# Performance work log

Measured on AMD Instinct MI355X. Metric: run time of the kernel, lower is better.

Reference implementation:

```python
import jax, jax.numpy as jnp
import numpy as np
from jax import lax


def setup_inputs() -> dict:
    key = jax.random.key(0)
    k1, k2 = jax.random.split(key)
    B, C, H, W = 4, 64, 64, 64
    foreground = jax.random.normal(k1, (B, C, H, W), dtype=jnp.float32)
    masks = jax.random.uniform(k2, (B, 1, H, W), dtype=jnp.float32)
    return {"foreground": foreground, "masks": masks}


def reference(foreground, masks):
    # First-call path of KnowledgeConsistentAttention (att_scores_prev is None).
    # patch_size=3 -> padding=1 around 1x1 dynamic kernels; propagate_size=3 -> 3x3 sum pool.
    B, C, H, W = foreground.shape
    P = H * W
    # Dynamic 1x1 kernels: one per spatial location, L2-normalized over channels.
    K = foreground.reshape(B, C, P).transpose(0, 2, 1)            # [B, P, C]
    norm = jnp.sqrt(jnp.sum(K * K, axis=2, keepdims=True))        # flatten(1).norm per kernel
    K = K / (norm + 1e-8)
    # conv2d with 1x1 kernels and padding=1 == GEMM over zero-padded input.
    Xpad = jnp.pad(foreground, ((0, 0), (0, 0), (1, 1), (1, 1)))  # [B, C, H+2, W+2]
    scores = jnp.einsum('bpc,bchw->bphw', K, Xpad)                # [B, P, H+2, W+2]
    # avg_pool2d(k=3, stride=1, pad=1) * 9 == zero-padded 3x3 sum pool.
    scores = lax.reduce_window(scores, jnp.float32(0.0), lax.add,
                               (1, 1, 3, 3), (1, 1, 1, 1), 'SAME')
    attn = jax.nn.softmax(scores, axis=1)                          # softmax over P kernels
    # conv_transpose2d with 1x1 kernels, padding=1 crops the border back to HxW.
    out = jnp.einsum('bphw,bpc->bchw', attn[:, :, 1:-1, 1:-1], K)  # [B, C, H, W]
    return out
```

## Files before the change

### kernel.cpp

```cpp
#include <hip/hip_runtime.h>
#include <hip/hip_bf16.h>
#include <math.h>

#define Bn 4
#define Cn 64
#define Pn 4096
#define QT 32
#define PBK 128
#define NITER (Pn / PBK)
#define LOG2E 1.4426950408889634f

typedef __attribute__((ext_vector_type(8))) short short8;
typedef __attribute__((ext_vector_type(4))) float float4v;
typedef unsigned short bfu;

__device__ __forceinline__ bfu f2bf(float x) {
    unsigned u = __float_as_uint(x);
    u = (u + 0x7fffu + ((u >> 16) & 1u)) >> 16;
    return (bfu)u;
}

__device__ __forceinline__ void async_load16(const bfu* g, bfu* l) {
    __builtin_amdgcn_global_load_lds(
        (const __attribute__((address_space(1))) unsigned int*)(const void*)g,
        (__attribute__((address_space(3))) unsigned int*)(void*)l,
        16, 0, 0);
}

__global__ __launch_bounds__(256) void prep_kernel(const float* __restrict__ fg,
                                                   bfu* __restrict__ Kpc,
                                                   bfu* __restrict__ Kcp,
                                                   float* __restrict__ S) {
    __shared__ float shbuf[64 * 64];
    int t = threadIdx.x;
    if (blockIdx.x < 512) {
        float* tile  = shbuf;
        float* rnorm = shbuf + 64 * 33;
        int b  = blockIdx.x >> 7;
        int p0 = (blockIdx.x & 127) << 5;
        const float* src = fg + (size_t)b * Cn * Pn + p0;
        #pragma unroll
        for (int i = 0; i < 8; ++i) {
            int idx = i * 256 + t;
            int c = idx >> 5, p = idx & 31;
            tile[c * 33 + p] = src[(size_t)c * Pn + p];
        }
        __syncthreads();
        if (t < 32) {
            float ss = 0.f;
            #pragma unroll
            for (int c = 0; c < 64; ++c) { float v = tile[c * 33 + t]; ss += v * v; }
            rnorm[t] = 1.0f / (sqrtf(ss) + 1e-8f);
        }
        __syncthreads();
        bfu* dpc = Kpc + ((size_t)b * Pn + p0) * Cn;
        #pragma unroll
        for (int i = 0; i < 8; ++i) {
            int idx = i * 256 + t;
            int p = idx >> 6, c = idx & 63;
            dpc[(size_t)p * Cn + c] = f2bf(tile[c * 33 + p] * rnorm[p]);
        }
        bfu* dcp = Kcp + (size_t)b * Cn * Pn + p0;
        #pragma unroll
        for (int i = 0; i < 8; ++i) {
            int idx = i * 256 + t;
            int c = idx >> 5, p = idx & 31;
            dcp[(size_t)c * Pn + p] = f2bf(tile[c * 33 + p] * rnorm[p]);
        }
    } else {
        float (*pl)[64] = (float(*)[64])shbuf;
        int bc = blockIdx.x - 512;
        const float* src = fg + (size_t)bc * Pn;
        float*       dst = S  + (size_t)bc * Pn;
        #pragma unroll
        for (int i = 0; i < 16; ++i) {
            int idx = i * 256 + t;
            pl[idx >> 6][idx & 63] = src[idx];
        }
        __syncthreads();
        #pragma unroll
        for (int i = 0; i < 16; ++i) {
            int idx = i * 256 + t;
            int h = idx >> 6, w = idx & 63;
            float s = 0.f;
            #pragma unroll
            for (int dh = -1; dh <= 1; ++dh) {
                int hh = h + dh;
                if (hh < 0 || hh >= 64) continue;
                #pragma unroll
                for (int dw = -1; dw <= 1; ++dw) {
                    int ww = w + dw;
                    if (ww < 0 || ww >= 64) continue;
                    s += pl[hh][ww];
                }
            }
            dst[idx] = s * LOG2E;
        }
    }
}

__global__ __launch_bounds__(256, 2) void flash_kernel(const bfu* __restrict__ Kpc,
                                                       const bfu* __restrict__ Kcp,
                                                       const float* __restrict__ S,
                                                       float* __restrict__ out) {
    __shared__ bfu Kpc_l[2][PBK * 64];
    __shared__ bfu Kcp_l[2][Cn * PBK];
    __shared__ bfu Sl[QT * 64];
    __shared__ bfu El[QT * PBK];
    __shared__ float wredl[4][QT];

    int b  = blockIdx.x >> 7;
    int q0 = (blockIdx.x & 127) * QT;
    int t  = threadIdx.x;
    int w = t >> 6, l = t & 63, lq = l & 15, quad = l >> 4;

    const float* Sg  = S   + (size_t)b * Cn * Pn;
    const bfu*   gpc = Kpc + (size_t)b * Pn * Cn;
    const bfu*   gcp = Kcp + (size_t)b * Cn * Pn;

    {
        int c = t >> 2, qq = (t & 3) * 8;
        const float* sp = &Sg[(size_t)c * Pn + q0 + qq];
        float4 v0 = *(const float4*)sp;
        float4 v1 = *(const float4*)(sp + 4);
        float vv[8] = {v0.x, v0.y, v0.z, v0.w, v1.x, v1.y, v1.z, v1.w};
        int ch = c >> 3, cl = c & 7;
        #pragma unroll
        for (int i = 0; i < 8; ++i) {
            int row = qq + i;
            Sl[row * 64 + ((ch ^ (row & 7)) << 3) + cl] = f2bf(vv[i]);
        }
    }

    #pragma unroll
    for (int j = 0; j < 4; ++j) {
        int ci = (w * 4 + j) * 64 + l;
        int row = ci >> 3, chp = ci & 7;
        async_load16(gpc + (size_t)row * Cn + ((chp ^ (row & 7)) << 3),
                     &Kpc_l[0][(w * 4 + j) * 512]);
    }
    #pragma unroll
    for (int j = 0; j < 4; ++j) {
        int ci = (w * 4 + j) * 64 + l;
        int c = ci >> 4, chp = ci & 15;
        async_load16(gcp + (size_t)c * Pn + ((chp ^ (c & 15)) << 3),
                     &Kcp_l[0][(w * 4 + j) * 512]);
    }
    __syncthreads();

    short8 bs[2][2];
    #pragma unroll
    for (int nt = 0; nt < 2; ++nt)
        #pragma unroll
        for (int ks = 0; ks < 2; ++ks) {
            int row = nt * 16 + lq;
            bs[nt][ks] = *(const short8*)&Sl[row * 64 + (((ks * 4 + quad) ^ (lq & 7)) << 3)];
        }

    float4v o[2];
    o[0] = (float4v){0.f, 0.f, 0.f, 0.f};
    o[1] = (float4v){0.f, 0.f, 0.f, 0.f};
    float lacc[2] = {0.f, 0.f};

    for (int pb = 0; pb < NITER; ++pb) {
        int cur = pb & 1;

        if (pb + 1 < NITER) {
            int nxt = cur ^ 1;
            const bfu* gpc_n = gpc + (size_t)(pb + 1) * PBK * Cn;
            const bfu* gcp_n = gcp + (size_t)(pb + 1) * PBK;
            #pragma unroll
            for (int j = 0; j < 4; ++j) {
                int ci = (w * 4 + j) * 64 + l;
                int row = ci >> 3, chp = ci & 7;
                async_load16(gpc_n + (size_t)row * Cn + ((chp ^ (row & 7)) << 3),
                             &Kpc_l[nxt][(w * 4 + j) * 512]);
            }
            #pragma unroll
            for (int j = 0; j < 4; ++j) {
                int ci = (w * 4 + j) * 64 + l;
                int c = ci >> 4, chp = ci & 15;
                async_load16(gcp_n + (size_t)c * Pn + ((chp ^ (c & 15)) << 3),
                             &Kcp_l[nxt][(w * 4 + j) * 512]);
            }
        }

        short8 af[2][2];
        #pragma unroll
        for (int mt = 0; mt < 2; ++mt)
            #pragma unroll
            for (int ks = 0; ks < 2; ++ks) {
                int row = w * 32 + mt * 16 + lq;
                af[mt][ks] = *(const short8*)&Kpc_l[cur][row * 64 + (((ks * 4 + quad) ^ (lq & 7)) << 3)];
            }
        float4v sc[2][2];
        #pragma unroll
        for (int mt = 0; mt < 2; ++mt)
            #pragma unroll
            for (int nt = 0; nt < 2; ++nt) {
                float4v acc = (float4v){0.f, 0.f, 0.f, 0.f};
                acc = __builtin_amdgcn_mfma_f32_16x16x32_bf16(af[mt][0], bs[nt][0], acc, 0, 0, 0);
                acc = __builtin_amdgcn_mfma_f32_16x16x32_bf16(af[mt][1], bs[nt][1], acc, 0, 0, 0);
                sc[mt][nt] = acc;
            }

        #pragma unroll
        for (int nt = 0; nt < 2; ++nt) {
            int row = nt * 16 + lq;
            #pragma unroll
            for (int mt = 0; mt < 2; ++mt) {
                float e0 = __builtin_amdgcn_exp2f(sc[mt][nt][0]);
                float e1 = __builtin_amdgcn_exp2f(sc[mt][nt][1]);
                float e2 = __builtin_amdgcn_exp2f(sc[mt][nt][2]);
                float e3 = __builtin_amdgcn_exp2f(sc[mt][nt][3]);
                lacc[nt] += (e0 + e1) + (e2 + e3);
                __hip_bfloat162 h01 = __float22bfloat162_rn(make_float2(e0, e1));
                __hip_bfloat162 h23 = __float22bfloat162_rn(make_float2(e2, e3));
                uint2 pk = make_uint2(*(unsigned*)&h01, *(unsigned*)&h23);
                int col = w * 32 + mt * 16 + quad * 4;
                int ch = (col >> 3) ^ (row & 15), cl = col & 7;
                *(uint2*)&El[row * PBK + ch * 8 + cl] = pk;
            }
        }
        __syncthreads();

        #pragma unroll
        for (int ks = 0; ks < 4; ++ks) {
            int rowA = w * 16 + lq;
            short8 ak = *(const short8*)&Kcp_l[cur][rowA * PBK + (((ks * 4 + quad) ^ lq) << 3)];
            #pragma unroll
            for (int nt = 0; nt < 2; ++nt) {
                int rowB = nt * 16 + lq;
                short8 bk = *(const short8*)&El[rowB * PBK + (((ks * 4 + quad) ^ lq) << 3)];
                o[nt] = __builtin_amdgcn_mfma_f32_16x16x32_bf16(ak, bk, o[nt], 0, 0, 0);
            }
        }
        __syncthreads();
    }

    #pragma unroll
    for (int nt = 0; nt < 2; ++nt) {
        lacc[nt] += __shfl_xor(lacc[nt], 16);
        lacc[nt] += __shfl_xor(lacc[nt], 32);
    }
    if (quad == 0) { wredl[w][lq] = lacc[0]; wredl[w][16 + lq] = lacc[1]; }
    __syncthreads();
    float* og = out + (size_t)b * Cn * Pn;
    #pragma unroll
    for (int nt = 0; nt < 2; ++nt) {
        int q = nt * 16 + lq;
        float linv = 1.0f / ((wredl[0][q] + wredl[1][q]) + (wredl[2][q] + wredl[3][q]));
        #pragma unroll
        for (int r = 0; r < 4; ++r) {
            int c = w * 16 + quad * 4 + r;
            og[(size_t)c * Pn + q0 + q] = o[nt][r] * linv;
        }
    }
}

extern "C" void kernel_launch(void* const* d_in, const int* in_sizes, int n_in,
                              void* d_out, int out_size, void* d_ws, size_t ws_size,
                              hipStream_t stream) {
    const float* fg = (const float*)d_in[0];
    float* out = (float*)d_out;
    bfu*   Kpc = (bfu*)d_ws;
    bfu*   Kcp = Kpc + (size_t)Bn * Pn * Cn;
    float* S   = (float*)(Kcp + (size_t)Bn * Pn * Cn);

    prep_kernel <<<768, 256, 0, stream>>>(fg, Kpc, Kcp, S);
    flash_kernel<<<Bn * 128, 256, 0, stream>>>(Kpc, Kcp, S, out);
}
```

Before: 107.1 us.

## Keep softmax probabilities in registers via shuffles, split-K PV across waves

Result: slower. 115.7 us (+8.0%).

```diff
diff --git a/kernel.cpp b/kernel.cpp
--- a/kernel.cpp
+++ b/kernel.cpp
@@ -103,11 +103,9 @@
                                                        const bfu* __restrict__ Kcp,
                                                        const float* __restrict__ S,
                                                        float* __restrict__ out) {
-    __shared__ bfu Kpc_l[2][PBK * 64];
-    __shared__ bfu Kcp_l[2][Cn * PBK];
-    __shared__ bfu Sl[QT * 64];
-    __shared__ bfu El[QT * PBK];
+    __shared__ __align__(16) bfu smem[2 * PBK * 64 + 2 * Cn * PBK + QT * 64];
     __shared__ float wredl[4][QT];
+    bfu* Sl = smem + 2 * PBK * 64 + 2 * Cn * PBK;
 
     int b  = blockIdx.x >> 7;
     int q0 = (blockIdx.x & 127) * QT;
@@ -137,14 +135,14 @@
         int ci = (w * 4 + j) * 64 + l;
         int row = ci >> 3, chp = ci & 7;
         async_load16(gpc + (size_t)row * Cn + ((chp ^ (row & 7)) << 3),
-                     &Kpc_l[0][(w * 4 + j) * 512]);
+                     smem + (w * 4 + j) * 512);
     }
     #pragma unroll
     for (int j = 0; j < 4; ++j) {
         int ci = (w * 4 + j) * 64 + l;
         int c = ci >> 4, chp = ci & 15;
         async_load16(gcp + (size_t)c * Pn + ((chp ^ (c & 15)) << 3),
-                     &Kcp_l[0][(w * 4 + j) * 512]);
+                     smem + 2 * PBK * 64 + (w * 4 + j) * 512);
     }
     __syncthreads();
 
@@ -157,16 +155,24 @@
             bs[nt][ks] = *(const short8*)&Sl[row * 64 + (((ks * 4 + quad) ^ (lq & 7)) << 3)];
         }
 
-    float4v o[2];
-    o[0] = (float4v){0.f, 0.f, 0.f, 0.f};
-    o[1] = (float4v){0.f, 0.f, 0.f, 0.f};
+    float4v o[4][2];
+    #pragma unroll
+    for (int ct = 0; ct < 4; ++ct)
+        #pragma unroll
+        for (int nt = 0; nt < 2; ++nt) o[ct][nt] = (float4v){0.f, 0.f, 0.f, 0.f};
     float lacc[2] = {0.f, 0.f};
 
+    int s0 = ((quad & 1) * 2) * 16 + lq;
+    int s1 = s0 + 16;
+    bool hi = quad >= 2;
+
     for (int pb = 0; pb < NITER; ++pb) {
-        int cur = pb & 1;
+        bfu* KpcC = smem + (pb & 1) * (PBK * 64);
+        bfu* KcpC = smem + 2 * PBK * 64 + (pb & 1) * (Cn * PBK);
 
         if (pb + 1 < NITER) {
-            int nxt = cur ^ 1;
+            bfu* KpcN = smem + ((pb + 1) & 1) * (PBK * 64);
+            bfu* KcpN = smem + 2 * PBK * 64 + ((pb + 1) & 1) * (Cn * PBK);
             const bfu* gpc_n = gpc + (size_t)(pb + 1) * PBK * Cn;
             const bfu* gcp_n = gcp + (size_t)(pb + 1) * PBK;
             #pragma unroll
@@ -174,14 +180,14 @@
                 int ci = (w * 4 + j) * 64 + l;
                 int row = ci >> 3, chp = ci & 7;
                 async_load16(gpc_n + (size_t)row * Cn + ((chp ^ (row & 7)) << 3),
-                             &Kpc_l[nxt][(w * 4 + j) * 512]);
+                             KpcN + (w * 4 + j) * 512);
             }
             #pragma unroll
             for (int j = 0; j < 4; ++j) {
                 int ci = (w * 4 + j) * 64 + l;
                 int c = ci >> 4, chp = ci & 15;
                 async_load16(gcp_n + (size_t)c * Pn + ((chp ^ (c & 15)) << 3),
-                             &Kcp_l[nxt][(w * 4 + j) * 512]);
+                             KcpN + (w * 4 + j) * 512);
             }
         }
 
@@ -191,7 +197,7 @@
             #pragma unroll
             for (int ks = 0; ks < 2; ++ks) {
                 int row = w * 32 + mt * 16 + lq;
-                af[mt][ks] = *(const short8*)&Kpc_l[cur][row * 64 + (((ks * 4 + quad) ^ (lq & 7)) << 3)];
+                af[mt][ks] = *(const short8*)&KpcC[row * 64 + (((ks * 4 + quad) ^ (lq & 7)) << 3)];
             }
         float4v sc[2][2];
         #pragma unroll
@@ -204,9 +210,9 @@
                 sc[mt][nt] = acc;
             }
 
-        #pragma unroll
-        for (int nt = 0; nt < 2; ++nt) {
-            int row = nt * 16 + lq;
+        unsigned pk[2][2][2];
+        #pragma unroll
+        for (int nt = 0; nt < 2; ++nt)
             #pragma unroll
             for (int mt = 0; mt < 2; ++mt) {
                 float e0 = __builtin_amdgcn_exp2f(sc[mt][nt][0]);
@@ -216,24 +222,37 @@
                 lacc[nt] += (e0 + e1) + (e2 + e3);
                 __hip_bfloat162 h01 = __float22bfloat162_rn(make_float2(e0, e1));
                 __hip_bfloat162 h23 = __float22bfloat162_rn(make_float2(e2, e3));
-                uint2 pk = make_uint2(*(unsigned*)&h01, *(unsigned*)&h23);
-                int col = w * 32 + mt * 16 + quad * 4;
-                int ch = (col >> 3) ^ (row & 15), cl = col & 7;
-                *(uint2*)&El[row * PBK + ch * 8 + cl] = pk;
-            }
-        }
-        __syncthreads();
-
-        #pragma unroll
-        for (int ks = 0; ks < 4; ++ks) {
-            int rowA = w * 16 + lq;
-            short8 ak = *(const short8*)&Kcp_l[cur][rowA * PBK + (((ks * 4 + quad) ^ lq) << 3)];
-            #pragma unroll
-            for (int nt = 0; nt < 2; ++nt) {
-                int rowB = nt * 16 + lq;
-                short8 bk = *(const short8*)&El[rowB * PBK + (((ks * 4 + quad) ^ lq) << 3)];
-                o[nt] = __builtin_amdgcn_mfma_f32_16x16x32_bf16(ak, bk, o[nt], 0, 0, 0);
-            }
+                pk[mt][nt][0] = *(unsigned*)&h01;
+                pk[mt][nt][1] = *(unsigned*)&h23;
+            }
+
+        short8 eb[2];
+        #pragma unroll
+        for (int nt = 0; nt < 2; ++nt) {
+            unsigned a, bq;
+            uint4 bw;
+            a  = (unsigned)__shfl((int)pk[0][nt][0], s0);
+            bq = (unsigned)__shfl((int)pk[1][nt][0], s0);
+            bw.x = hi ? bq : a;
+            a  = (unsigned)__shfl((int)pk[0][nt][1], s0);
+            bq = (unsigned)__shfl((int)pk[1][nt][1], s0);
+            bw.y = hi ? bq : a;
+            a  = (unsigned)__shfl((int)pk[0][nt][0], s1);
+            bq = (unsigned)__shfl((int)pk[1][nt][0], s1);
+            bw.z = hi ? bq : a;
+            a  = (unsigned)__shfl((int)pk[0][nt][1], s1);
+            bq = (unsigned)__shfl((int)pk[1][nt][1], s1);
+            bw.w = hi ? bq : a;
+            eb[nt] = *(short8*)&bw;
+        }
+
+        #pragma unroll
+        for (int ct = 0; ct < 4; ++ct) {
+            int row = ct * 16 + lq;
+            short8 ak = *(const short8*)&KcpC[row * PBK + (((4 * w + quad) ^ (row & 15)) << 3)];
+            #pragma unroll
+            for (int nt = 0; nt < 2; ++nt)
+                o[ct][nt] = __builtin_amdgcn_mfma_f32_16x16x32_bf16(ak, eb[nt], o[ct][nt], 0, 0, 0);
         }
         __syncthreads();
     }
@@ -245,16 +264,30 @@
     }
     if (quad == 0) { wredl[w][lq] = lacc[0]; wredl[w][16 + lq] = lacc[1]; }
     __syncthreads();
-    float* og = out + (size_t)b * Cn * Pn;
+    float linv[2];
     #pragma unroll
     for (int nt = 0; nt < 2; ++nt) {
         int q = nt * 16 + lq;
-        float linv = 1.0f / ((wredl[0][q] + wredl[1][q]) + (wredl[2][q] + wredl[3][q]));
-        #pragma unroll
-        for (int r = 0; r < 4; ++r) {
-            int c = w * 16 + quad * 4 + r;
-            og[(size_t)c * Pn + q0 + q] = o[nt][r] * linv;
-        }
+        linv[nt] = 1.0f / ((wredl[0][q] + wredl[1][q]) + (wredl[2][q] + wredl[3][q]));
+    }
+
+    float* Ol = (float*)smem;
+    #pragma unroll
+    for (int ct = 0; ct < 4; ++ct)
+        #pragma unroll
+        for (int nt = 0; nt < 2; ++nt)
+            #pragma unroll
+            for (int r = 0; r < 4; ++r)
+                Ol[(w * 64 + ct * 16 + quad * 4 + r) * 33 + nt * 16 + lq] = o[ct][nt][r] * linv[nt];
+    __syncthreads();
+    float* og = out + (size_t)b * Cn * Pn;
+    #pragma unroll
+    for (int i = 0; i < 8; ++i) {
+        int idx = i * 256 + t;
+        int c = idx >> 5, q = idx & 31;
+        float v = (Ol[(c)*33 + q] + Ol[(64 + c) * 33 + q]) +
+                  (Ol[(128 + c) * 33 + q] + Ol[(192 + c) * 33 + q]);
+        og[(size_t)c * Pn + q0 + q] = v;
     }
 }
 
```

## Use 8 waves per block with split-K PV GEMM and LDS reduction

Applied to the files above, without the earlier changes.

Measured after the change: 102.9 us. 3.9% less time.

```diff
diff --git a/kernel.cpp b/kernel.cpp
--- a/kernel.cpp
+++ b/kernel.cpp
@@ -99,15 +99,14 @@
     }
 }
 
-__global__ __launch_bounds__(256, 2) void flash_kernel(const bfu* __restrict__ Kpc,
+__global__ __launch_bounds__(512, 2) void flash_kernel(const bfu* __restrict__ Kpc,
                                                        const bfu* __restrict__ Kcp,
                                                        const float* __restrict__ S,
                                                        float* __restrict__ out) {
-    __shared__ bfu Kpc_l[2][PBK * 64];
-    __shared__ bfu Kcp_l[2][Cn * PBK];
-    __shared__ bfu Sl[QT * 64];
-    __shared__ bfu El[QT * PBK];
-    __shared__ float wredl[4][QT];
+    __shared__ __align__(16) bfu smem[2 * PBK * 64 + 2 * Cn * PBK + QT * 64 + QT * PBK];
+    __shared__ float wredl[8][QT];
+    bfu* Sl = smem + 2 * PBK * 64 + 2 * Cn * PBK;
+    bfu* El = Sl + QT * 64;
 
     int b  = blockIdx.x >> 7;
     int q0 = (blockIdx.x & 127) * QT;
@@ -119,32 +118,32 @@
     const bfu*   gcp = Kcp + (size_t)b * Cn * Pn;
 
     {
-        int c = t >> 2, qq = (t & 3) * 8;
+        int c = t >> 3, qq = (t & 7) * 4;
         const float* sp = &Sg[(size_t)c * Pn + q0 + qq];
         float4 v0 = *(const float4*)sp;
-        float4 v1 = *(const float4*)(sp + 4);
-        float vv[8] = {v0.x, v0.y, v0.z, v0.w, v1.x, v1.y, v1.z, v1.w};
+        float vv[4] = {v0.x, v0.y, v0.z, v0.w};
         int ch = c >> 3, cl = c & 7;
         #pragma unroll
-        for (int i = 0; i < 8; ++i) {
+        for (int i = 0; i < 4; ++i) {
             int row = qq + i;
             Sl[row * 64 + ((ch ^ (row & 7)) << 3) + cl] = f2bf(vv[i]);
         }
     }
 
     #pragma unroll
-    for (int j = 0; j < 4; ++j) {
-        int ci = (w * 4 + j) * 64 + l;
+    for (int j = 0; j < 2; ++j) {
+        int g = j * 8 + w;
+        int ci = g * 64 + l;
         int row = ci >> 3, chp = ci & 7;
-        async_load16(gpc + (size_t)row * Cn + ((chp ^ (row & 7)) << 3),
-                     &Kpc_l[0][(w * 4 + j) * 512]);
-    }
-    #pragma unroll
-    for (int j = 0; j < 4; ++j) {
-        int ci = (w * 4 + j) * 64 + l;
+        async_load16(gpc + (size_t)row * Cn + ((chp ^ (row & 7)) << 3), smem + g * 512);
+    }
+    #pragma unroll
+    for (int j = 0; j < 2; ++j) {
+        int g = j * 8 + w;
+        int ci = g * 64 + l;
         int c = ci >> 4, chp = ci & 15;
         async_load16(gcp + (size_t)c * Pn + ((chp ^ (c & 15)) << 3),
-                     &Kcp_l[0][(w * 4 + j) * 512]);
+                     smem + 2 * PBK * 64 + g * 512);
     }
     __syncthreads();
 
@@ -162,76 +161,76 @@
     o[1] = (float4v){0.f, 0.f, 0.f, 0.f};
     float lacc[2] = {0.f, 0.f};
 
+    int h  = w >> 2;
+    int ca = (w & 3) * 16;
+
     for (int pb = 0; pb < NITER; ++pb) {
-        int cur = pb & 1;
+        bfu* KpcC = smem + (pb & 1) * (PBK * 64);
+        bfu* KcpC = smem + 2 * PBK * 64 + (pb & 1) * (Cn * PBK);
 
         if (pb + 1 < NITER) {
-            int nxt = cur ^ 1;
+            bfu* KpcN = smem + ((pb + 1) & 1) * (PBK * 64);
+            bfu* KcpN = smem + 2 * PBK * 64 + ((pb + 1) & 1) * (Cn * PBK);
             const bfu* gpc_n = gpc + (size_t)(pb + 1) * PBK * Cn;
             const bfu* gcp_n = gcp + (size_t)(pb + 1) * PBK;
             #pragma unroll
-            for (int j = 0; j < 4; ++j) {
-                int ci = (w * 4 + j) * 64 + l;
+            for (int j = 0; j < 2; ++j) {
+                int g = j * 8 + w;
+                int ci = g * 64 + l;
                 int row = ci >> 3, chp = ci & 7;
                 async_load16(gpc_n + (size_t)row * Cn + ((chp ^ (row & 7)) << 3),
-                             &Kpc_l[nxt][(w * 4 + j) * 512]);
-            }
-            #pragma unroll
-            for (int j = 0; j < 4; ++j) {
-                int ci = (w * 4 + j) * 64 + l;
+                             KpcN + g * 512);
+            }
+            #pragma unroll
+            for (int j = 0; j < 2; ++j) {
+                int g = j * 8 + w;
+                int ci = g * 64 + l;
                 int c = ci >> 4, chp = ci & 15;
                 async_load16(gcp_n + (size_t)c * Pn + ((chp ^ (c & 15)) << 3),
-                             &Kcp_l[nxt][(w * 4 + j) * 512]);
-            }
-        }
-
-        short8 af[2][2];
-        #pragma unroll
-        for (int mt = 0; mt < 2; ++mt)
-            #pragma unroll
-            for (int ks = 0; ks < 2; ++ks) {
-                int row = w * 32 + mt * 16 + lq;
-                af[mt][ks] = *(const short8*)&Kpc_l[cur][row * 64 + (((ks * 4 + quad) ^ (lq & 7)) << 3)];
-            }
-        float4v sc[2][2];
-        #pragma unroll
-        for (int mt = 0; mt < 2; ++mt)
-            #pragma unroll
-            for (int nt = 0; nt < 2; ++nt) {
-                float4v acc = (float4v){0.f, 0.f, 0.f, 0.f};
-                acc = __builtin_amdgcn_mfma_f32_16x16x32_bf16(af[mt][0], bs[nt][0], acc, 0, 0, 0);
-                acc = __builtin_amdgcn_mfma_f32_16x16x32_bf16(af[mt][1], bs[nt][1], acc, 0, 0, 0);
-                sc[mt][nt] = acc;
-            }
+                             KcpN + g * 512);
+            }
+        }
+
+        short8 af[2];
+        #pragma unroll
+        for (int ks = 0; ks < 2; ++ks) {
+            int row = w * 16 + lq;
+            af[ks] = *(const short8*)&KpcC[row * 64 + (((ks * 4 + quad) ^ (lq & 7)) << 3)];
+        }
+        float4v sc[2];
+        #pragma unroll
+        for (int nt = 0; nt < 2; ++nt) {
+            float4v acc = (float4v){0.f, 0.f, 0.f, 0.f};
+            acc = __builtin_amdgcn_mfma_f32_16x16x32_bf16(af[0], bs[nt][0], acc, 0, 0, 0);
+            acc = __builtin_amdgcn_mfma_f32_16x16x32_bf16(af[1], bs[nt][1], acc, 0, 0, 0);
+            sc[nt] = acc;
+        }
 
         #pragma unroll
         for (int nt = 0; nt < 2; ++nt) {
             int row = nt * 16 + lq;
-            #pragma unroll
-            for (int mt = 0; mt < 2; ++mt) {
-                float e0 = __builtin_amdgcn_exp2f(sc[mt][nt][0]);
-                float e1 = __builtin_amdgcn_exp2f(sc[mt][nt][1]);
-                float e2 = __builtin_amdgcn_exp2f(sc[mt][nt][2]);
-                float e3 = __builtin_amdgcn_exp2f(sc[mt][nt][3]);
-                lacc[nt] += (e0 + e1) + (e2 + e3);
-                __hip_bfloat162 h01 = __float22bfloat162_rn(make_float2(e0, e1));
-                __hip_bfloat162 h23 = __float22bfloat162_rn(make_float2(e2, e3));
-                uint2 pk = make_uint2(*(unsigned*)&h01, *(unsigned*)&h23);
-                int col = w * 32 + mt * 16 + quad * 4;
-                int ch = (col >> 3) ^ (row & 15), cl = col & 7;
-                *(uint2*)&El[row * PBK + ch * 8 + cl] = pk;
-            }
-        }
-        __syncthreads();
-
-        #pragma unroll
-        for (int ks = 0; ks < 4; ++ks) {
-            int rowA = w * 16 + lq;
-            short8 ak = *(const short8*)&Kcp_l[cur][rowA * PBK + (((ks * 4 + quad) ^ lq) << 3)];
+            float e0 = __builtin_amdgcn_exp2f(sc[nt][0]);
+            float e1 = __builtin_amdgcn_exp2f(sc[nt][1]);
+            float e2 = __builtin_amdgcn_exp2f(sc[nt][2]);
+            float e3 = __builtin_amdgcn_exp2f(sc[nt][3]);
+            lacc[nt] += (e0 + e1) + (e2 + e3);
+            __hip_bfloat162 h01 = __float22bfloat162_rn(make_float2(e0, e1));
+            __hip_bfloat162 h23 = __float22bfloat162_rn(make_float2(e2, e3));
+            uint2 pk = make_uint2(*(unsigned*)&h01, *(unsigned*)&h23);
+            int col = w * 16 + quad * 4;
+            int ch = (col >> 3) ^ (row & 15), cl = col & 7;
+            *(uint2*)&El[row * PBK + ch * 8 + cl] = pk;
+        }
+        __syncthreads();
+
+        #pragma unroll
+        for (int ks = 0; ks < 2; ++ks) {
+            int rowA = ca + lq;
+            short8 ak = *(const short8*)&KcpC[rowA * PBK + (((8 * h + ks * 4 + quad) ^ (rowA & 15)) << 3)];
             #pragma unroll
             for (int nt = 0; nt < 2; ++nt) {
                 int rowB = nt * 16 + lq;
-                short8 bk = *(const short8*)&El[rowB * PBK + (((ks * 4 + quad) ^ lq) << 3)];
+                short8 bk = *(const short8*)&El[rowB * PBK + (((8 * h + ks * 4 + quad) ^ (rowB & 15)) << 3)];
                 o[nt] = __builtin_amdgcn_mfma_f32_16x16x32_bf16(ak, bk, o[nt], 0, 0, 0);
             }
         }
@@ -244,17 +243,24 @@
         lacc[nt] += __shfl_xor(lacc[nt], 32);
     }
     if (quad == 0) { wredl[w][lq] = lacc[0]; wredl[w][16 + lq] = lacc[1]; }
+
+    float* Ol = (float*)smem;
+    __syncthreads();
+    #pragma unroll
+    for (int nt = 0; nt < 2; ++nt)
+        #pragma unroll
+        for (int r = 0; r < 4; ++r)
+            Ol[(h * 64 + ca + quad * 4 + r) * 33 + nt * 16 + lq] = o[nt][r];
     __syncthreads();
     float* og = out + (size_t)b * Cn * Pn;
     #pragma unroll
-    for (int nt = 0; nt < 2; ++nt) {
-        int q = nt * 16 + lq;
-        float linv = 1.0f / ((wredl[0][q] + wredl[1][q]) + (wredl[2][q] + wredl[3][q]));
-        #pragma unroll
-        for (int r = 0; r < 4; ++r) {
-            int c = w * 16 + quad * 4 + r;
-            og[(size_t)c * Pn + q0 + q] = o[nt][r] * linv;
-        }
+    for (int i = 0; i < 4; ++i) {
+        int idx = i * 512 + t;
+        int c = idx >> 5, q = idx & 31;
+        float lsum = ((wredl[0][q] + wredl[1][q]) + (wredl[2][q] + wredl[3][q])) +
+                     ((wredl[4][q] + wredl[5][q]) + (wredl[6][q] + wredl[7][q]));
+        float v = (Ol[c * 33 + q] + Ol[(64 + c) * 33 + q]) / lsum;
+        og[(size_t)c * Pn + q0 + q] = v;
     }
 }
 
@@ -268,5 +274,5 @@
     float* S   = (float*)(Kcp + (size_t)Bn * Pn * Cn);
 
     prep_kernel <<<768, 256, 0, stream>>>(fg, Kpc, Kcp, S);
-    flash_kernel<<<Bn * 128, 256, 0, stream>>>(Kpc, Kcp, S, out);
-}
+    flash_kernel<<<Bn * 128, 512, 0, stream>>>(Kpc, Kcp, S, out);
+}
```
